# Kernel tuning notes

Hardware: AMD Instinct MI355X
Metric: run time of the kernel (lower is better)

Reference implementation:

```python
import jax, jax.numpy as jnp
import numpy as np

B, N, P2, D, L, K = 256, 256, 64, 128, 2, 9  # batch, nodes, patch^2, embed_dim, vig blocks, knn edges
FFN = 4 * D


def _ln(x, g, b, eps=1e-5):
    m = jnp.mean(x, -1, keepdims=True)
    v = jnp.mean((x - m) ** 2, -1, keepdims=True)
    return (x - m) / jnp.sqrt(v + eps) * g + b


def _lrelu(x):
    return jnp.where(x >= 0, x, 0.01 * x)


def _vig_block(x, mask, mf, fc1_w, fc1_b, conv_w, conv_b, fc2_w, fc2_b, f1_w, f1_b, f2_w, f2_b):
    # Grapher: fc1 -> dynamic kNN -> max-relative graph conv -> fc2, residual
    sc = x
    h = x @ fc1_w + fc1_b  # [B,N,D]
    # pairwise squared distances in feature space; masked nodes excluded as neighbors
    x2 = jnp.sum(h * h, -1)
    d2 = x2[:, :, None] + x2[:, None, :] - 2.0 * jnp.einsum('bnd,bmd->bnm', h, h)
    d2 = jnp.where(mask[:, None, :], d2, 1e10)
    _, idx = jax.lax.top_k(-d2, K)  # [B,N,K] nearest-neighbor indices (non-diff)
    Bq, Nq, Dq = h.shape
    hj = jnp.take_along_axis(h, idx.reshape(Bq, Nq * K, 1), axis=1).reshape(Bq, Nq, K, Dq)
    vj = jnp.take_along_axis(mask, idx.reshape(Bq, Nq * K), axis=1).reshape(Bq, Nq, K)
    rel = jnp.where(vj[..., None], hj - h[:, :, None, :], -1e9)
    mrel = jnp.where(vj.any(2)[..., None], rel.max(2), 0.0)  # max-relative aggregation
    h = _lrelu(jnp.concatenate([h, mrel], -1) @ conv_w + conv_b)
    x = (h @ fc2_w + fc2_b) + sc
    # FFN, residual (drop_path = identity at eval)
    sc = x
    x = _lrelu(x @ f1_w + f1_b) @ f2_w + f2_b + sc
    return x * mf


def setup_inputs() -> dict:
    key = jax.random.key(0)
    ks = jax.random.split(key, 32)
    s = 0.02
    d = {
        'nodes_batch': jax.random.normal(ks[0], (B, N, P2), jnp.float32),
        'node_mask': jax.random.randint(ks[1], (B, N), 0, 2) > 0,
        'emb_w1': jax.random.normal(ks[2], (P2, 2 * D), jnp.float32) * s,
        'emb_b1': jnp.zeros((2 * D,), jnp.float32),
        'emb_ln1_g': jnp.ones((2 * D,), jnp.float32),
        'emb_ln1_b': jnp.zeros((2 * D,), jnp.float32),
        'emb_w2': jax.random.normal(ks[3], (2 * D, D), jnp.float32) * s,
        'emb_b2': jnp.zeros((D,), jnp.float32),
        'emb_ln2_g': jnp.ones((D,), jnp.float32),
        'emb_ln2_b': jnp.zeros((D,), jnp.float32),
        'vig_fc1_w': jax.random.normal(ks[4], (L, D, D), jnp.float32) * s,
        'vig_fc1_b': jnp.zeros((L, D), jnp.float32),
        'vig_conv_w': jax.random.normal(ks[5], (L, 2 * D, D), jnp.float32) * s,
        'vig_conv_b': jnp.zeros((L, D), jnp.float32),
        'vig_fc2_w': jax.random.normal(ks[6], (L, D, D), jnp.float32) * s,
        'vig_fc2_b': jnp.zeros((L, D), jnp.float32),
        'vig_ffn1_w': jax.random.normal(ks[7], (L, D, FFN), jnp.float32) * s,
        'vig_ffn1_b': jnp.zeros((L, FFN), jnp.float32),
        'vig_ffn2_w': jax.random.normal(ks[8], (L, FFN, D), jnp.float32) * s,
        'vig_ffn2_b': jnp.zeros((L, D), jnp.float32),
        'out_w1': jax.random.normal(ks[9], (D, 512), jnp.float32) * s,
        'out_b1': jnp.zeros((512,), jnp.float32),
        'out_w2': jax.random.normal(ks[10], (512, 2048), jnp.float32) * s,
        'out_b2': jnp.zeros((2048,), jnp.float32),
    }
    return d


def reference(nodes_batch, node_mask, emb_w1, emb_b1, emb_ln1_g, emb_ln1_b, emb_w2, emb_b2,
              emb_ln2_g, emb_ln2_b, vig_fc1_w, vig_fc1_b, vig_conv_w, vig_conv_b,
              vig_fc2_w, vig_fc2_b, vig_ffn1_w, vig_ffn1_b, vig_ffn2_w, vig_ffn2_b,
              out_w1, out_b1, out_w2, out_b2):
    mf = node_mask[..., None].astype(nodes_batch.dtype)  # [B,N,1]
    # node embed MLP
    x = _lrelu(_ln(nodes_batch @ emb_w1 + emb_b1, emb_ln1_g, emb_ln1_b))
    x = _ln(x @ emb_w2 + emb_b2, emb_ln2_g, emb_ln2_b)
    x = x * mf
    for l in range(L):
        x = _vig_block(x, node_mask, mf,
                       vig_fc1_w[l], vig_fc1_b[l], vig_conv_w[l], vig_conv_b[l],
                       vig_fc2_w[l], vig_fc2_b[l], vig_ffn1_w[l], vig_ffn1_b[l],
                       vig_ffn2_w[l], vig_ffn2_b[l])
    # masked mean pool
    sum_feat = (x * mf).sum(1)
    num_feat = jnp.maximum(mf.sum(1), 1.0)
    g = sum_feat / num_feat
    return _lrelu(g @ out_w1 + out_b1) @ out_w2 + out_b2
```

## Files before the change

### kernel.cpp

```cpp
#include <hip/hip_runtime.h>
#include <cstdint>

#define BB    256
#define NNODE 256
#define PP2   64
#define DD    128
#define LLAY  2
#define KNN   9
#define FFND  512
#define BNROWS (BB*NNODE)

#define LRELU_(v) ((v) >= 0.f ? (v) : 0.01f*(v))

enum { ACT_NONE = 0, ACT_LRELU = 1 };

typedef short  short8_t  __attribute__((ext_vector_type(8)));
typedef float  f32x4     __attribute__((ext_vector_type(4)));
typedef unsigned short us4 __attribute__((ext_vector_type(4)));
typedef unsigned short us8 __attribute__((ext_vector_type(8)));

__device__ inline unsigned short f2bf(float x) {
    unsigned u = __float_as_uint(x);
    unsigned r = (u + 0x7FFFu + ((u >> 16) & 1u)) >> 16;
    return (unsigned short)r;
}
__device__ inline float bf2f(unsigned short h) {
    return __uint_as_float(((unsigned)h) << 16);
}

__device__ inline void gload16(const void* src, void* dst) {
    __builtin_amdgcn_global_load_lds(
        (const __attribute__((address_space(1))) void*)src,
        (__attribute__((address_space(3))) void*)dst, 16, 0, 0);
}

template<int ROWS, int WAVES>
__device__ inline void stage64g(const unsigned short* __restrict__ g, size_t rowbase,
                                int Kel, int k0, unsigned short* lds, int w, int lane)
{
    constexpr int PER = (ROWS*128/1024) / WAVES;
    #pragma unroll
    for (int i = 0; i < PER; ++i) {
        const int inst = w + i*WAVES;
        const unsigned o  = (unsigned)inst*1024u + (unsigned)lane*16u;
        const int      r  = (int)(o >> 7);
        const unsigned cb = o & 127u;
        const unsigned cs = cb ^ ((unsigned)(r & 7) << 4);
        gload16((const char*)(g + (rowbase + (size_t)r)*(size_t)Kel + k0) + cs,
                (char*)lds + (size_t)inst*1024u);
    }
}

__device__ inline short8_t frag64(const unsigned short* lds, int r, int cb) {
    return *reinterpret_cast<const short8_t*>(
        (const char*)lds + (size_t)r*128 + (unsigned)(cb ^ ((r & 7) << 4)));
}

__device__ inline us8 read8sw(const unsigned short* lds, int r, unsigned cb) {
    return *reinterpret_cast<const us8*>(
        (const char*)lds + (size_t)r*128 + (cb ^ ((unsigned)(r & 7) << 4)));
}

__device__ inline unsigned grp16_min_u32(unsigned v) {
    unsigned t;
    t = (unsigned)__builtin_amdgcn_update_dpp(-1, (int)v, 0xB1,  0xF, 0xF, false); v = t < v ? t : v;
    t = (unsigned)__builtin_amdgcn_update_dpp(-1, (int)v, 0x4E,  0xF, 0xF, false); v = t < v ? t : v;
    t = (unsigned)__builtin_amdgcn_update_dpp(-1, (int)v, 0x124, 0xF, 0xF, false); v = t < v ? t : v;
    t = (unsigned)__builtin_amdgcn_update_dpp(-1, (int)v, 0x128, 0xF, 0xF, false); v = t < v ? t : v;
    return v;
}

__device__ inline float dpp_rowsum16(float v) {
    float t;
    t = __uint_as_float((unsigned)__builtin_amdgcn_update_dpp(0, (int)__float_as_uint(v), 0x111, 0xF, 0xF, false)); v += t;
    t = __uint_as_float((unsigned)__builtin_amdgcn_update_dpp(0, (int)__float_as_uint(v), 0x112, 0xF, 0xF, false)); v += t;
    t = __uint_as_float((unsigned)__builtin_amdgcn_update_dpp(0, (int)__float_as_uint(v), 0x114, 0xF, 0xF, false)); v += t;
    t = __uint_as_float((unsigned)__builtin_amdgcn_update_dpp(0, (int)__float_as_uint(v), 0x118, 0xF, 0xF, false)); v += t;
    return v;
}

#define WAITB0  { asm volatile("s_waitcnt vmcnt(0)" ::: "memory");  __builtin_amdgcn_s_barrier(); asm volatile("" ::: "memory"); }
#define WAITB4  { asm volatile("s_waitcnt vmcnt(4)" ::: "memory");  __builtin_amdgcn_s_barrier(); asm volatile("" ::: "memory"); }
#define WAITB6  { asm volatile("s_waitcnt vmcnt(6)" ::: "memory");  __builtin_amdgcn_s_barrier(); asm volatile("" ::: "memory"); }
#define WAITBL4 { asm volatile("s_waitcnt vmcnt(4) lgkmcnt(0)" ::: "memory"); __builtin_amdgcn_s_barrier(); asm volatile("" ::: "memory"); }

template<int ACT, bool RES, bool MASK, bool OUTF, bool OUTB, bool OUTS>
__global__ __launch_bounds__(256)
void bgemm_k(const unsigned short* __restrict__ A,
             const unsigned short* __restrict__ W,
             const float* __restrict__ bias,
             const float* __restrict__ resp,
             const int* __restrict__ mask,
             float* __restrict__ Cf, unsigned short* __restrict__ Cb,
             unsigned short* Ohi, unsigned short* Olo,
             int M, int N, int K)
{
    __shared__ __align__(16) unsigned short As[128*64];
    __shared__ __align__(16) unsigned short Bs[128*64];

    const int tid  = threadIdx.x;
    const int lane = tid & 63;
    const int w    = tid >> 6;
    const int wr   = w >> 1, wc = w & 1;
    const int row0 = blockIdx.x * 128;
    const int col0 = blockIdx.y * 128;
    const int l15  = lane & 15;
    const int ko   = lane >> 4;

    f32x4 acc[4][4];
    #pragma unroll
    for (int m = 0; m < 4; ++m)
        #pragma unroll
        for (int n = 0; n < 4; ++n) acc[m][n] = (f32x4){0.f,0.f,0.f,0.f};

    for (int k0 = 0; k0 < K; k0 += 64) {
        stage64g<128,4>(A, (size_t)row0, K, k0, As, w, lane);
        stage64g<128,4>(W, (size_t)col0, K, k0, Bs, w, lane);
        __syncthreads();
        #pragma unroll
        for (int ks = 0; ks < 2; ++ks) {
            short8_t aF[4], bF[4];
            #pragma unroll
            for (int m = 0; m < 4; ++m)
                aF[m] = frag64(As, wr*64 + m*16 + l15, ks*64 + ko*16);
            #pragma unroll
            for (int n = 0; n < 4; ++n)
                bF[n] = frag64(Bs, wc*64 + n*16 + l15, ks*64 + ko*16);
            #pragma unroll
            for (int m = 0; m < 4; ++m)
                #pragma unroll
                for (int n = 0; n < 4; ++n)
                    acc[m][n] = __builtin_amdgcn_mfma_f32_16x16x32_bf16(aF[m], bF[n], acc[m][n], 0, 0, 0);
        }
        __syncthreads();
    }

    #pragma unroll
    for (int m = 0; m < 4; ++m) {
        const int rbase = row0 + wr*64 + m*16 + ko*4;
        #pragma unroll
        for (int n = 0; n < 4; ++n) {
            const int col = col0 + wc*64 + n*16 + l15;
            const float bv = bias[col];
            #pragma unroll
            for (int r = 0; r < 4; ++r) {
                const int row = rbase + r;
                float v = acc[m][n][r] + bv;
                if constexpr (ACT == ACT_LRELU) v = LRELU_(v);
                if constexpr (RES)  v += resp[(size_t)row*N + col];
                if constexpr (MASK) v *= (mask[row] != 0) ? 1.f : 0.f;
                if constexpr (OUTF) Cf[(size_t)row*N + col] = v;
                if constexpr (OUTB) Cb[(size_t)row*N + col] = f2bf(v);
                if constexpr (OUTS) {
                    unsigned short h = f2bf(v);
                    Ohi[(size_t)row*N + col] = h;
                    Olo[(size_t)row*N + col] = f2bf(v - bf2f(h));
                }
            }
        }
    }
}

template<int WR, int WC, bool DO_LRELU, bool MASKMUL, int MODE, bool AF32>
__global__ __launch_bounds__(WR*WC*64)
void bgemm_ln_k(const void* __restrict__ Ap,
                const unsigned short* __restrict__ W,
                const float* __restrict__ bias,
// ... 71 lines not shown
        __syncthreads();
    }

    float bv[4];
    #pragma unroll
    for (int n = 0; n < 4; ++n) bv[n] = bias[wc*64 + n*16 + l15];
    #pragma unroll
    for (int m = 0; m < 4; ++m)
        #pragma unroll
        for (int n = 0; n < 4; ++n)
            #pragma unroll
            for (int r = 0; r < 4; ++r) acc[m][n][r] += bv[n];

    #pragma unroll
    for (int m = 0; m < 4; ++m) {
        #pragma unroll
        for (int r = 0; r < 4; ++r) {
            float s = acc[m][0][r] + acc[m][1][r] + acc[m][2][r] + acc[m][3][r];
            float q = acc[m][0][r]*acc[m][0][r] + acc[m][1][r]*acc[m][1][r]
                    + acc[m][2][r]*acc[m][2][r] + acc[m][3][r]*acc[m][3][r];
            s = dpp_rowsum16(s);
            q = dpp_rowsum16(q);
            if (l15 == 15) {
                int rl = wr*64 + m*16 + ko*4 + r;
                red_s[wc][rl] = s;
                red_q[wc][rl] = q;
            }
        }
    }
    __syncthreads();
    if (tid < BM) {
        float s = 0.f, q = 0.f;
        #pragma unroll
        for (int c2 = 0; c2 < WC; ++c2) { s += red_s[c2][tid]; q += red_q[c2][tid]; }
        float mu  = s * (1.0f/BN);
        float var = q * (1.0f/BN) - mu*mu;
        mu_l[tid] = mu;
        rs_l[tid] = rsqrtf(fmaxf(var, 0.f) + 1e-5f);
    }
    __syncthreads();

    float gm[4], bt[4];
    #pragma unroll
    for (int n = 0; n < 4; ++n) {
        int col = wc*64 + n*16 + l15;
        gm[n] = gam[col]; bt[n] = bet[col];
    }
    #pragma unroll
    for (int m = 0; m < 4; ++m) {
        #pragma unroll
        for (int r = 0; r < 4; ++r) {
            const int rl  = wr*64 + m*16 + ko*4 + r;
            const int row = row0 + rl;
            const float mu = mu_l[rl], rs = rs_l[rl];
            float mf = 1.f;
            if constexpr (MASKMUL) mf = (mask[row] != 0) ? 1.f : 0.f;
            #pragma unroll
            for (int n = 0; n < 4; ++n) {
                const int col = wc*64 + n*16 + l15;
                float y = (acc[m][n][r] - mu) * rs * gm[n] + bt[n];
                if constexpr (DO_LRELU) y = LRELU_(y);
                if constexpr (MASKMUL)  y *= mf;
                if constexpr (MODE == 1) {
                    ((unsigned short*)outv)[(size_t)row*BN + col] = f2bf(y);
                } else {
                    unsigned short h = f2bf(y);
                    ohi[(size_t)row*BN + col] = h;
                    olo[(size_t)row*BN + col] = f2bf(y - bf2f(h));
                }
            }
        }
    }
}

__global__ __launch_bounds__(1024)
void fc1_dist_topk_gather_k(const unsigned short* __restrict__ xhi,
                            const unsigned short* __restrict__ xlo,
                            const unsigned short* __restrict__ Whi,
                            const unsigned short* __restrict__ Wlo,
                            const float* __restrict__ fc1b,
                            const int* __restrict__ mask,
                            unsigned short* __restrict__ cat)
{
    __shared__ __align__(16) unsigned short BsH[2][NNODE*64];
    __shared__ __align__(16) unsigned short BsL[2][NNODE*64];
    __shared__ __align__(16) unsigned short Ws[128*64];
    __shared__ float x2s[NNODE];
    __shared__ unsigned char idx_s[NNODE*KNN];
    __shared__ unsigned char msk_s[NNODE];

    const int b    = blockIdx.x;
    const int tid  = threadIdx.x;
    const int lane = tid & 63;
    const int w    = tid >> 6;
    const int l15  = lane & 15;
    const int g    = lane >> 4;

    const unsigned short* Xhi = xhi + (size_t)b*NNODE*DD;
    const unsigned short* Xlo = xlo + (size_t)b*NNODE*DD;
    const int* mkb = mask + b*NNODE;

    stage64g<NNODE,16>(Xhi, 0, DD, 0,  &BsH[0][0], w, lane);
    stage64g<NNODE,16>(Xhi, 0, DD, 64, &BsH[1][0], w, lane);
    stage64g<NNODE,16>(Xlo, 0, DD, 0,  &BsL[0][0], w, lane);
    stage64g<NNODE,16>(Xlo, 0, DD, 64, &BsL[1][0], w, lane);
    if (tid < NNODE) msk_s[tid] = (mkb[tid] != 0) ? 1 : 0;
    __syncthreads();

    const int arow = w*16 + l15;

    f32x4 hacc[8];
    #pragma unroll
    for (int n = 0; n < 8; ++n) hacc[n] = (f32x4){0.f,0.f,0.f,0.f};

    #pragma unroll
    for (int wp = 0; wp < 4; ++wp) {
        const unsigned short* Wsrc = (wp < 2) ? Whi : Wlo;
        const int kt = wp & 1;
        stage64g<128,16>(Wsrc, 0, DD, kt*64, Ws, w, lane);
        __syncthreads();
        const int nAv = (wp < 2) ? 2 : 1;
        for (int av = 0; av < nAv; ++av) {
            const unsigned short* At = (av == 0) ? &BsH[kt][0] : &BsL[kt][0];
            #pragma unroll
            for (int ks = 0; ks < 2; ++ks) {
                short8_t aF = frag64(At, arow, ks*64 + g*16);
                #pragma unroll
                for (int n = 0; n < 8; ++n) {
                    short8_t bF = frag64(Ws, n*16 + l15, ks*64 + g*16);
                    hacc[n] = __builtin_amdgcn_mfma_f32_16x16x32_bf16(aF, bF, hacc[n], 0, 0, 0);
                }
            }
        }
        __syncthreads();
    }

    {
        float qr[4] = {0.f, 0.f, 0.f, 0.f};
        #pragma unroll
        for (int n = 0; n < 8; ++n) {
            const int col = n*16 + l15;
            const float bv = fc1b[col];
            const int kt = col >> 6;
            const unsigned bc = (unsigned)((col & 63) * 2);
            #pragma unroll
            for (int r = 0; r < 4; ++r) {
                const int row = w*16 + g*4 + r;
                float v = hacc[n][r] + bv;
                unsigned short hh = f2bf(v);
                unsigned short hl = f2bf(v - bf2f(hh));
                const unsigned off = (unsigned)(row*128) + (bc ^ ((unsigned)(row & 7) << 4));
                *(unsigned short*)((char*)&BsH[kt][0] + off) = hh;
                *(unsigned short*)((char*)&BsL[kt][0] + off) = hl;
                float vv = bf2f(hh) + bf2f(hl);
                qr[r] += vv*vv;
            }
        }
        #pragma unroll
        for (int r = 0; r < 4; ++r) {
            float q = dpp_rowsum16(qr[r]);
            if (l15 == 15) x2s[w*16 + g*4 + r] = q;
        }
    }
    __syncthreads();

    f32x4 acc[16];
    #pragma unroll
    for (int n = 0; n < 16; ++n) acc[n] = (f32x4){0.f,0.f,0.f,0.f};

    __builtin_amdgcn_s_setprio(1);
    #pragma unroll
    for (int kt = 0; kt < 2; ++kt) {
        #pragma unroll
        for (int ks = 0; ks < 2; ++ks) {
            short8_t aH = frag64(&BsH[kt][0], arow, ks*64 + g*16);
            short8_t aL = frag64(&BsL[kt][0], arow, ks*64 + g*16);
            #pragma unroll
            for (int n = 0; n < 16; ++n) {
                int brow = n*16 + l15;
                short8_t bH = frag64(&BsH[kt][0], brow, ks*64 + g*16);
                short8_t bL = frag64(&BsL[kt][0], brow, ks*64 + g*16);
                acc[n] = __builtin_amdgcn_mfma_f32_16x16x32_bf16(aH, bH, acc[n], 0, 0, 0);
                acc[n] = __builtin_amdgcn_mfma_f32_16x16x32_bf16(aL, bH, acc[n], 0, 0, 0);
                acc[n] = __builtin_amdgcn_mfma_f32_16x16x32_bf16(aH, bL, acc[n], 0, 0, 0);
            }
        }
    }
    __builtin_amdgcn_s_setprio(0);

    float x2c[16]; unsigned mk[16];
    #pragma unroll
    for (int n = 0; n < 16; ++n) {
        int col = n*16 + l15;
        x2c[n] = x2s[col];
        mk[n]  = (unsigned)msk_s[col];
    }

    #pragma unroll
    for (int r = 0; r < 4; ++r) {
        const int lrow = w*16 + g*4 + r;
        const float x2r = x2s[lrow];
        unsigned key[16];
        #pragma unroll
        for (int n = 0; n < 16; ++n) {
            float v = x2r + x2c[n] - 2.0f*acc[n][r];
            if (!mk[n]) v = 1e10f;
            unsigned u = __float_as_uint(v);
            u = (u & 0x80000000u) ? ~u : (u | 0x80000000u);
            key[n] = (u & 0xFFFFFF00u) | (unsigned)(n*16 + l15);
        }
        for (int it = 0; it < KNN; ++it) {
            unsigned a0 = key[0]  < key[1]  ? key[0]  : key[1];
            unsigned a1 = key[2]  < key[3]  ? key[2]  : key[3];
            unsigned a2 = key[4]  < key[5]  ? key[4]  : key[5];
            unsigned a3 = key[6]  < key[7]  ? key[6]  : key[7];
            unsigned a4 = key[8]  < key[9]  ? key[8]  : key[9];
            unsigned a5 = key[10] < key[11] ? key[10] : key[11];
            unsigned a6 = key[12] < key[13] ? key[12] : key[13];
            unsigned a7 = key[14] < key[15] ? key[14] : key[15];
            unsigned b0 = a0 < a1 ? a0 : a1;
            unsigned b1 = a2 < a3 ? a2 : a3;
            unsigned b2 = a4 < a5 ? a4 : a5;
            unsigned b3 = a6 < a7 ? a6 : a7;
            unsigned c0 = b0 < b1 ? b0 : b1;
            unsigned c1 = b2 < b3 ? b2 : b3;
            unsigned lmin = c0 < c1 ? c0 : c1;
            unsigned gmin = grp16_min_u32(lmin);
            if (l15 == 0) idx_s[lrow*KNN + it] = (unsigned char)(gmin & 0xFFu);
            #pragma unroll
            for (int n = 0; n < 16; ++n)
                if (key[n] == gmin) key[n] = 0xFFFFFFFFu;
        }
    }

    const int gi = lane & 7;
    const unsigned cb = (unsigned)(gi * 16);
    #pragma unroll
    for (int kt = 0; kt < 2; ++kt) {
        #pragma unroll
        for (int p = 0; p < 2; ++p) {
            const int rl = w*16 + p*8 + (lane >> 3);
            us8 h8 = read8sw(&BsH[kt][0], rl, cb);
            us8 l8 = read8sw(&BsL[kt][0], rl, cb);
            float hi[8], m[8];
            #pragma unroll
            for (int d = 0; d < 8; ++d) { hi[d] = bf2f(h8[d]) + bf2f(l8[d]); m[d] = -1e9f; }
            bool any = false;
            #pragma unroll
            for (int q = 0; q < KNN; ++q) {
                int j = idx_s[rl*KNN + q];
                if (msk_s[j]) {
                    any = true;
                    us8 a = read8sw(&BsH[kt][0], j, cb);
                    us8 o = read8sw(&BsL[kt][0], j, cb);
                    #pragma unroll
                    for (int d = 0; d < 8; ++d)
                        m[d] = fmaxf(m[d], bf2f(a[d]) + bf2f(o[d]) - hi[d]);
                }
            }
            us8 o1, o2;
            #pragma unroll
            for (int d = 0; d < 8; ++d) {
                o1[d] = f2bf(hi[d]);
                o2[d] = any ? f2bf(m[d]) : (unsigned short)0;
            }
            const size_t rowbase = (size_t)(b*NNODE + rl)*(2*DD);
            const int c0 = kt*64 + gi*8;
            *reinterpret_cast<us8*>(&cat[rowbase + c0])      = o1;
            *reinterpret_cast<us8*>(&cat[rowbase + DD + c0]) = o2;
        }
    }
}

__global__ __launch_bounds__(256)
void conv_ffn_k(const unsigned short* __restrict__ cat,
                const unsigned short* __restrict__ Wc,
                const float* __restrict__ cb,
                const unsigned short* __restrict__ W2c,
                const float* __restrict__ fb,
                const unsigned short* __restrict__ W1,
                const float* __restrict__ b1,
                const unsigned short* __restrict__ W2f,
                const float* __restrict__ b2,
                const int* __restrict__ mask,
                unsigned short* xhi,
                unsigned short* xlo)
{
    __shared__ __align__(16) unsigned short Bs[3][128*64];
    __shared__ __align__(16) unsigned short h2s[2][64*64];
    __shared__ __align__(16) unsigned short Xs[2][64*64];

    const int tid  = threadIdx.x;
    const int lane = tid & 63;
    const int w    = tid >> 6;
    const int row0 = blockIdx.x * 64;
    const int l15  = lane & 15;
    const int ko   = lane >> 4;

    auto issueB = [&](int t) {
        unsigned short* buf = &Bs[t % 3][0];
        if (t < 4)      stage64g<128,4>(Wc,  0, 256, t*64, buf, w, lane);
        else if (t < 6) stage64g<128,4>(W2c, 0, 128, (t-4)*64, buf, w, lane);
        else {
            int c = (t-6) >> 2, j = (t-6) & 3;
            if (j < 2) stage64g<128,4>(W1, (size_t)(c*128), DD, j*64, buf, w, lane);
            else       stage64g<128,4>(W2f, 0, FFND, c*128 + (j-2)*64, buf, w, lane);
        }
    };

    #define MM8(ATILE, BTILE, ACC)                                              \
        { __builtin_amdgcn_s_setprio(1);                                        \
          _Pragma("unroll")                                                     \
          for (int ks = 0; ks < 2; ++ks) {                                      \
            short8_t aF[4], bF[2];                                              \
            _Pragma("unroll")                                                   \
            for (int m = 0; m < 4; ++m) aF[m] = frag64(ATILE, m*16 + l15, ks*64 + ko*16); \
            _Pragma("unroll")                                                   \
            for (int n = 0; n < 2; ++n) bF[n] = frag64(BTILE, w*32 + n*16 + l15, ks*64 + ko*16); \
            _Pragma("unroll")                                                   \
            for (int m = 0; m < 4; ++m)                                         \
              _Pragma("unroll")                                                 \
              for (int n = 0; n < 2; ++n)                                       \
                ACC[m][n] = __builtin_amdgcn_mfma_f32_16x16x32_bf16(aF[m], bF[n], ACC[m][n], 0, 0, 0); } \
          __builtin_amdgcn_s_setprio(0); }

    #define H2WRITE(ACC, BPTR, DST)                                             \
        { const int kt_ = w >> 1;                                               \
          _Pragma("unroll")                                                     \
          for (int n = 0; n < 2; ++n) {                                         \
            const int col_ = w*32 + n*16 + l15;                                 \
            const float bv_ = (BPTR)[col_];                                     \
            const unsigned bc_ = (unsigned)(((w & 1)*32 + n*16 + l15) * 2);     \
            _Pragma("unroll")                                                   \
            for (int m = 0; m < 4; ++m)                                         \
              _Pragma("unroll")                                                 \
              for (int r = 0; r < 4; ++r) {                                     \
                const int row_ = m*16 + ko*4 + r;                               \
                float v_ = LRELU_(ACC[m][n][r] + bv_);                          \
                *(unsigned short*)((char*)&(DST)[kt_][0] + row_*128             \
                    + (bc_ ^ ((unsigned)(row_ & 7) << 4))) = f2bf(v_); } } }

    stage64g<64,4>(cat, (size_t)row0, 256, 0,  &Xs[0][0], w, lane);
    issueB(0);
    stage64g<64,4>(cat, (size_t)row0, 256, 64, &Xs[1][0], w, lane);
    issueB(1);

    f32x4 accc[4][2];
    #pragma unroll
    for (int m = 0; m < 4; ++m)
        #pragma unroll
        for (int n = 0; n < 2; ++n) accc[m][n] = (f32x4){0.f,0.f,0.f,0.f};

    WAITB6;
    issueB(2);
    MM8(&Xs[0][0], &Bs[0][0], accc);

    WAITB4;
    stage64g<64,4>(cat, (size_t)row0, 256, 128, &Xs[0][0], w, lane);
    issueB(3);
    MM8(&Xs[1][0], &Bs[1][0], accc);

    WAITB4;
    stage64g<64,4>(cat, (size_t)row0, 256, 192, &Xs[1][0], w, lane);
    issueB(4);
    MM8(&Xs[0][0], &Bs[2][0], accc);

    WAITB4;
    issueB(5);
    MM8(&Xs[1][0], &Bs[0][0], accc);
    H2WRITE(accc, cb, h2s);

    f32x4 accx[4][2];
    #pragma unroll
    for (int m = 0; m < 4; ++m)
        #pragma unroll
        for (int n = 0; n < 2; ++n) accx[m][n] = (f32x4){0.f,0.f,0.f,0.f};

    WAITBL4;
    issueB(6);
    MM8(&h2s[0][0], &Bs[1][0], accx);

    WAITB4;
    issueB(7);
    MM8(&h2s[1][0], &Bs[2][0], accx);
    float xn[4][2][4];
    {
        const int kt = w >> 1;
        #pragma unroll
        for (int n = 0; n < 2; ++n) {
            const int col = w*32 + n*16 + l15;
            const float bv = fb[col];
            const unsigned bc = (unsigned)(((w & 1)*32 + n*16 + l15) * 2);
            #pragma unroll
            for (int m = 0; m < 4; ++m) {
                #pragma unroll
                for (int r = 0; r < 4; ++r) {
                    const int row = m*16 + ko*4 + r;
                    const size_t gix = (size_t)(row0 + row)*DD + col;
                    float res = bf2f(xhi[gix]) + bf2f(xlo[gix]);
                    float v = accx[m][n][r] + bv + res;
                    xn[m][n][r] = v;
                    *(unsigned short*)((char*)&Xs[kt][0] + row*128
                        + (bc ^ ((unsigned)(row & 7) << 4))) = f2bf(v);
                }
            }
        }
    }

    f32x4 acc2[4][2];
    #pragma unroll
    for (int m = 0; m < 4; ++m)
        #pragma unroll
        for (int n = 0; n < 2; ++n) acc2[m][n] = (f32x4){0.f,0.f,0.f,0.f};

    #pragma unroll
    for (int c = 0; c < 4; ++c) {
        const int tb = 6 + c*4;
        f32x4 acc1[4][2];
        #pragma unroll
        for (int m = 0; m < 4; ++m)
            #pragma unroll
            for (int n = 0; n < 2; ++n) acc1[m][n] = (f32x4){0.f,0.f,0.f,0.f};

        if (c == 0) { WAITBL4; } else { WAITB4; }
        if (tb+2 <= 21) issueB(tb+2);
        MM8(&Xs[0][0], &Bs[tb % 3][0], acc1);

        WAITB4;
        if (tb+3 <= 21) issueB(tb+3);
        MM8(&Xs[1][0], &Bs[(tb+1) % 3][0], acc1);
        H2WRITE(acc1, b1 + c*128, h2s);

        WAITBL4;
        if (tb+4 <= 21) issueB(tb+4);
        MM8(&h2s[0][0], &Bs[(tb+2) % 3][0], acc2);

        if (c == 3) { WAITB0; } else { WAITB4; }
        if (tb+5 <= 21) issueB(tb+5);
        MM8(&h2s[1][0], &Bs[(tb+3) % 3][0], acc2);
    }

    #pragma unroll
    for (int m = 0; m < 4; ++m) {
        const int rbase = row0 + m*16 + ko*4;
        #pragma unroll
        for (int n = 0; n < 2; ++n) {
            const int col = w*32 + n*16 + l15;
            const float bv = b2[col];
            #pragma unroll
            for (int r = 0; r < 4; ++r) {
                const int row = rbase + r;
                float v = acc2[m][n][r] + bv + xn[m][n][r];
                v *= (mask[row] != 0) ? 1.f : 0.f;
                unsigned short h = f2bf(v);
                xhi[(size_t)row*DD + col] = h;
                xlo[(size_t)row*DD + col] = f2bf(v - bf2f(h));
            }
        }
    }
    #undef MM8
    #undef H2WRITE
}

__global__ __launch_bounds__(128)
void pool_k(const unsigned short* __restrict__ xhi, const unsigned short* __restrict__ xlo,
            const int* __restrict__ mask,
            float* __restrict__ g, unsigned short* __restrict__ gbf)
{
    const int b = blockIdx.x, c = threadIdx.x;
    float s = 0.f; int cnt = 0;
    for (int n = 0; n < NNODE; ++n) {
        const size_t ix = ((size_t)b*NNODE + n)*DD + c;
        s += bf2f(xhi[ix]) + bf2f(xlo[ix]);
        cnt += (mask[b*NNODE + n] != 0) ? 1 : 0;
    }
    float v = s / fmaxf((float)cnt, 1.0f);
    g[b*DD + c] = v;
    gbf[b*DD + c] = f2bf(v);
}

__global__ __launch_bounds__(256)
void prep_all_k(const float* __restrict__ emb_w1, const float* __restrict__ emb_w2,
                const float* __restrict__ conv_w, const float* __restrict__ fc2_w,
                const float* __restrict__ f1_w,   const float* __restrict__ f2_w,
                const float* __restrict__ fc1_w,  const float* __restrict__ ow1,
                const float* __restrict__ ow2,
                unsigned short* __restrict__ emb_w1t, unsigned short* __restrict__ emb_w2t,
                unsigned short* __restrict__ conv_wt, unsigned short* __restrict__ fc2_wt,
                unsigned short* __restrict__ ffn1_wt, unsigned short* __restrict__ ffn2_wt,
                unsigned short* __restrict__ fc1_wthi, unsigned short* __restrict__ fc1_wtlo,
                unsigned short* __restrict__ ow1t, unsigned short* __restrict__ ow2t)
{
    __shared__ float tile[32][33];
    const int tx = threadIdx.x & 31, ty = threadIdx.x >> 5;

    int bid = blockIdx.x;
    const float* src = nullptr; unsigned short* dst = nullptr; unsigned short* dlo = nullptr;
    int K = 0, N = 0;
    do {
        if (bid < 16)  { src = emb_w1; dst = emb_w1t; K = 64;  N = 256; break; }  bid -= 16;
        if (bid < 32)  { src = emb_w2; dst = emb_w2t; K = 256; N = 128; break; }  bid -= 32;
        if (bid < 64)  { int l = bid >> 5; bid &= 31;
                         src = conv_w + (size_t)l*256*128; dst = conv_wt + (size_t)l*128*256;
                         K = 256; N = 128; break; }                               bid -= 64;
        if (bid < 32)  { int l = bid >> 4; bid &= 15;
                         src = fc2_w + (size_t)l*128*128; dst = fc2_wt + (size_t)l*128*128;
                         K = 128; N = 128; break; }                               bid -= 32;
        if (bid < 128) { int l = bid >> 6; bid &= 63;
                         src = f1_w + (size_t)l*128*512; dst = ffn1_wt + (size_t)l*512*128;
                         K = 128; N = 512; break; }                               bid -= 128;
        if (bid < 128) { int l = bid >> 6; bid &= 63;
                         src = f2_w + (size_t)l*512*128; dst = ffn2_wt + (size_t)l*128*512;
                         K = 512; N = 128; break; }                               bid -= 128;
        if (bid < 32)  { int l = bid >> 4; bid &= 15;
                         src = fc1_w + (size_t)l*128*128;
                         dst = fc1_wthi + (size_t)l*128*128; dlo = fc1_wtlo + (size_t)l*128*128;
                         K = 128; N = 128; break; }                               bid -= 32;
        if (bid < 64)  { src = ow1; dst = ow1t; K = 128; N = 512; break; }        bid -= 64;
        { src = ow2; dst = ow2t; K = 512; N = 2048; }
    } while (0);

    const int nbx = N / 32;
    const int bx = bid % nbx, by = bid / nbx;
    const int k0 = by*32, n0 = bx*32;

    #pragma unroll
    for (int i = ty; i < 32; i += 8)
        tile[i][tx] = src[(size_t)(k0+i)*N + n0+tx];
    __syncthreads();
    #pragma unroll
// ... 3 lines not shown
        dst[(size_t)(n0+i)*K + k0+tx] = h;
        if (dlo) dlo[(size_t)(n0+i)*K + k0+tx] = f2bf(v - bf2f(h));
    }
}

extern "C" void kernel_launch(void* const* d_in, const int* in_sizes, int n_in,
                              void* d_out, int out_size, void* d_ws, size_t ws_size,
                              hipStream_t stream)
{
    const float* nodes  = (const float*)d_in[0];
    const int*   maskp  = (const int*)  d_in[1];
    const float* emb_w1 = (const float*)d_in[2];
    const float* emb_b1 = (const float*)d_in[3];
    const float* ln1_g  = (const float*)d_in[4];
    const float* ln1_b  = (const float*)d_in[5];
    const float* emb_w2 = (const float*)d_in[6];
    const float* emb_b2 = (const float*)d_in[7];
    const float* ln2_g  = (const float*)d_in[8];
    const float* ln2_b  = (const float*)d_in[9];
    const float* fc1_w  = (const float*)d_in[10];
    const float* fc1_b  = (const float*)d_in[11];
    const float* conv_w = (const float*)d_in[12];
    const float* conv_b = (const float*)d_in[13];
    const float* fc2_w  = (const float*)d_in[14];
    const float* fc2_b  = (const float*)d_in[15];
    const float* f1_w   = (const float*)d_in[16];
    const float* f1_b   = (const float*)d_in[17];
    const float* f2_w   = (const float*)d_in[18];
    const float* f2_b   = (const float*)d_in[19];
    const float* ow1    = (const float*)d_in[20];
    const float* ob1    = (const float*)d_in[21];
    const float* ow2    = (const float*)d_in[22];
    const float* ob2    = (const float*)d_in[23];
    float* out = (float*)d_out;

    char* base = (char*)d_ws;
    char*  H   = base + (size_t)BNROWS*DD*4;
    char*  BIG = H + (size_t)BNROWS*DD*4;
    float*          g     = (float*)(BIG + (size_t)BNROWS*2*DD*4);
    unsigned short* g_bf  = (unsigned short*)(g + BB*DD);
    unsigned short* hid2_bf = g_bf + BB*DD;
    unsigned short* wbuf  = hid2_bf + BB*FFND;

    unsigned short* x_hi   = (unsigned short*)H;
    unsigned short* x_lo   = x_hi + (size_t)BNROWS*DD;
    unsigned short* t256_bf= (unsigned short*)base;
    unsigned short* cat_bf = (unsigned short*)BIG;

    unsigned short* emb_w1t  = wbuf;
    unsigned short* emb_w2t  = emb_w1t + 256*64;
    unsigned short* conv_wt  = emb_w2t + 128*256;
    unsigned short* fc2_wt   = conv_wt + 2*128*256;
    unsigned short* ffn1_wt  = fc2_wt  + 2*128*128;
    unsigned short* ffn2_wt  = ffn1_wt + 2*512*128;
    unsigned short* fc1_wthi = ffn2_wt + 2*128*512;
    unsigned short* fc1_wtlo = fc1_wthi + 2*128*128;
    unsigned short* ow1t     = fc1_wtlo + 2*128*128;
    unsigned short* ow2t     = ow1t + 512*128;

    const dim3 blk(256);

    prep_all_k<<<1520, blk, 0, stream>>>(
        emb_w1, emb_w2, conv_w, fc2_w, f1_w, f2_w, fc1_w, ow1, ow2,
        emb_w1t, emb_w2t, conv_wt, fc2_wt, ffn1_wt, ffn2_wt,
        fc1_wthi, fc1_wtlo, ow1t, ow2t);

    bgemm_ln_k<2,4,true,false,1,true>
        <<<dim3(BNROWS/128), dim3(512), 0, stream>>>
        (nodes, emb_w1t, emb_b1, ln1_g, ln1_b, nullptr, t256_bf, nullptr, nullptr, PP2);
    bgemm_ln_k<2,2,false,true,2,false>
        <<<dim3(BNROWS/128), dim3(256), 0, stream>>>
        (t256_bf, emb_w2t, emb_b2, ln2_g, ln2_b, maskp, nullptr, x_hi, x_lo, 2*DD);

    for (int l = 0; l < LLAY; ++l) {
        const float* fc1b = fc1_b + (size_t)l*DD;
        const float* cb   = conv_b + (size_t)l*DD;
        const float* fc2b = fc2_b + (size_t)l*DD;
        const float* b1   = f1_b + (size_t)l*FFND;
        const float* b2   = f2_b + (size_t)l*DD;

        fc1_dist_topk_gather_k<<<dim3(BB), dim3(1024), 0, stream>>>
            (x_hi, x_lo, fc1_wthi + (size_t)l*DD*DD, fc1_wtlo + (size_t)l*DD*DD,
             fc1b, maskp, cat_bf);
        conv_ffn_k<<<dim3(BNROWS/64), blk, 0, stream>>>
            (cat_bf, conv_wt + (size_t)l*DD*2*DD, cb,
             fc2_wt + (size_t)l*DD*DD, fc2b,
             ffn1_wt + (size_t)l*FFND*DD, b1,
             ffn2_wt + (size_t)l*DD*FFND, b2, maskp,
             x_hi, x_lo);
    }

    pool_k<<<BB, 128, 0, stream>>>(x_hi, x_lo, maskp, g, g_bf);
    bgemm_k<ACT_LRELU,false,false,false,true,false>
        <<<dim3(BB/128, 512/128), blk, 0, stream>>>
        (g_bf, ow1t, ob1, nullptr, nullptr, nullptr, hid2_bf, nullptr, nullptr, BB, 512, DD);
    bgemm_k<ACT_NONE,false,false,true,false,false>
        <<<dim3(BB/128, 2048/128), blk, 0, stream>>>
        (hid2_bf, ow2t, ob2, nullptr, nullptr, out, nullptr, nullptr, nullptr, BB, 2048, 512);
}
```

Measured before the change: 273.1 us.

## Convert fc1 output to fp32 LDS layout and skip fully masked top-k rows

The hi/lo bf16 LDS buffers are merged into one array. After the distance MFMA, the fc1 output is rebuilt as fp32 and rewritten in a swizzled fp32 layout that reuses the same LDS. The gather then reads fp32 directly and takes the max of neighbor values before subtracting the center, which cuts conversions and LDS reads per neighbor. Top-k selection is also skipped for row groups where all rows are masked out. This adds an extra barrier and an LDS rewrite pass. Subtracting after the max gives a slightly different rounding order from the reference.

```diff
diff --git a/kernel.cpp b/kernel.cpp
--- a/kernel.cpp
+++ b/kernel.cpp
@@ -54,11 +54,6 @@
 __device__ inline short8_t frag64(const unsigned short* lds, int r, int cb) {
     return *reinterpret_cast<const short8_t*>(
         (const char*)lds + (size_t)r*128 + (unsigned)(cb ^ ((r & 7) << 4)));
-}
-
-__device__ inline us8 read8sw(const unsigned short* lds, int r, unsigned cb) {
-    return *reinterpret_cast<const us8*>(
-        (const char*)lds + (size_t)r*128 + (cb ^ ((unsigned)(r & 7) << 4)));
 }
 
 __device__ inline unsigned grp16_min_u32(unsigned v) {
@@ -320,8 +315,7 @@
                             const int* __restrict__ mask,
                             unsigned short* __restrict__ cat)
 {
-    __shared__ __align__(16) unsigned short BsH[2][NNODE*64];
-    __shared__ __align__(16) unsigned short BsL[2][NNODE*64];
+    __shared__ __align__(16) unsigned short BUF[4][NNODE*64];
     __shared__ __align__(16) unsigned short Ws[128*64];
     __shared__ float x2s[NNODE];
     __shared__ unsigned char idx_s[NNODE*KNN];
@@ -338,10 +332,10 @@
     const unsigned short* Xlo = xlo + (size_t)b*NNODE*DD;
     const int* mkb = mask + b*NNODE;
 
-    stage64g<NNODE,16>(Xhi, 0, DD, 0,  &BsH[0][0], w, lane);
-    stage64g<NNODE,16>(Xhi, 0, DD, 64, &BsH[1][0], w, lane);
-    stage64g<NNODE,16>(Xlo, 0, DD, 0,  &BsL[0][0], w, lane);
-    stage64g<NNODE,16>(Xlo, 0, DD, 64, &BsL[1][0], w, lane);
+    stage64g<NNODE,16>(Xhi, 0, DD, 0,  &BUF[0][0], w, lane);
+    stage64g<NNODE,16>(Xhi, 0, DD, 64, &BUF[1][0], w, lane);
+    stage64g<NNODE,16>(Xlo, 0, DD, 0,  &BUF[2][0], w, lane);
+    stage64g<NNODE,16>(Xlo, 0, DD, 64, &BUF[3][0], w, lane);
     if (tid < NNODE) msk_s[tid] = (mkb[tid] != 0) ? 1 : 0;
     __syncthreads();
 
@@ -359,7 +353,7 @@
         __syncthreads();
         const int nAv = (wp < 2) ? 2 : 1;
         for (int av = 0; av < nAv; ++av) {
-            const unsigned short* At = (av == 0) ? &BsH[kt][0] : &BsL[kt][0];
+            const unsigned short* At = (av == 0) ? &BUF[kt][0] : &BUF[2+kt][0];
             #pragma unroll
             for (int ks = 0; ks < 2; ++ks) {
                 short8_t aF = frag64(At, arow, ks*64 + g*16);
@@ -388,8 +382,8 @@
                 unsigned short hh = f2bf(v);
                 unsigned short hl = f2bf(v - bf2f(hh));
                 const unsigned off = (unsigned)(row*128) + (bc ^ ((unsigned)(row & 7) << 4));
-                *(unsigned short*)((char*)&BsH[kt][0] + off) = hh;
-                *(unsigned short*)((char*)&BsL[kt][0] + off) = hl;
+                *(unsigned short*)((char*)&BUF[kt][0]   + off) = hh;
+                *(unsigned short*)((char*)&BUF[2+kt][0] + off) = hl;
                 float vv = bf2f(hh) + bf2f(hl);
                 qr[r] += vv*vv;
             }
@@ -411,13 +405,13 @@
     for (int kt = 0; kt < 2; ++kt) {
         #pragma unroll
         for (int ks = 0; ks < 2; ++ks) {
-            short8_t aH = frag64(&BsH[kt][0], arow, ks*64 + g*16);
-            short8_t aL = frag64(&BsL[kt][0], arow, ks*64 + g*16);
+            short8_t aH = frag64(&BUF[kt][0],   arow, ks*64 + g*16);
+            short8_t aL = frag64(&BUF[2+kt][0], arow, ks*64 + g*16);
             #pragma unroll
             for (int n = 0; n < 16; ++n) {
                 int brow = n*16 + l15;
-                short8_t bH = frag64(&BsH[kt][0], brow, ks*64 + g*16);
-                short8_t bL = frag64(&BsL[kt][0], brow, ks*64 + g*16);
+                short8_t bH = frag64(&BUF[kt][0],   brow, ks*64 + g*16);
+                short8_t bL = frag64(&BUF[2+kt][0], brow, ks*64 + g*16);
                 acc[n] = __builtin_amdgcn_mfma_f32_16x16x32_bf16(aH, bH, acc[n], 0, 0, 0);
                 acc[n] = __builtin_amdgcn_mfma_f32_16x16x32_bf16(aL, bH, acc[n], 0, 0, 0);
                 acc[n] = __builtin_amdgcn_mfma_f32_16x16x32_bf16(aH, bL, acc[n], 0, 0, 0);
@@ -434,8 +428,35 @@
         mk[n]  = (unsigned)msk_s[col];
     }
 
+    {
+        float sv[32];
+        const int r0  = tid >> 2;
+        const int cb4 = tid & 3;
+        const int kt  = cb4 >> 1;
+        const unsigned base = (unsigned)((cb4 & 1) * 64);
+        const unsigned sw = (unsigned)(r0 & 7) << 4;
+        #pragma unroll
+        for (int i = 0; i < 4; ++i) {
+            const unsigned bc = (base + (unsigned)(i*16)) ^ sw;
+            us8 hh = *reinterpret_cast<const us8*>((const char*)&BUF[kt][0]   + r0*128 + bc);
+            us8 hl = *reinterpret_cast<const us8*>((const char*)&BUF[2+kt][0] + r0*128 + bc);
+            #pragma unroll
+            for (int d = 0; d < 8; ++d) sv[i*8+d] = bf2f(hh[d]) + bf2f(hl[d]);
+        }
+        __syncthreads();
+        char* S = (char*)&BUF[0][0];
+        #pragma unroll
+        for (int i = 0; i < 8; ++i) {
+            const unsigned bo = ((unsigned)(cb4*128 + i*16)) ^ sw;
+            *reinterpret_cast<f32x4*>(S + (size_t)r0*512 + bo) =
+                (f32x4){sv[i*4], sv[i*4+1], sv[i*4+2], sv[i*4+3]};
+        }
+    }
+
     #pragma unroll
     for (int r = 0; r < 4; ++r) {
+        const int rb = w*16 + r;
+        if ((msk_s[rb] | msk_s[rb+4] | msk_s[rb+8] | msk_s[rb+12]) == 0) continue;
         const int lrow = w*16 + g*4 + r;
         const float x2r = x2s[lrow];
         unsigned key[16];
@@ -470,42 +491,51 @@
                 if (key[n] == gmin) key[n] = 0xFFFFFFFFu;
         }
     }
-
-    const int gi = lane & 7;
-    const unsigned cb = (unsigned)(gi * 16);
-    #pragma unroll
-    for (int kt = 0; kt < 2; ++kt) {
-        #pragma unroll
-        for (int p = 0; p < 2; ++p) {
-            const int rl = w*16 + p*8 + (lane >> 3);
-            us8 h8 = read8sw(&BsH[kt][0], rl, cb);
-            us8 l8 = read8sw(&BsL[kt][0], rl, cb);
-            float hi[8], m[8];
-            #pragma unroll
-            for (int d = 0; d < 8; ++d) { hi[d] = bf2f(h8[d]) + bf2f(l8[d]); m[d] = -1e9f; }
-            bool any = false;
-            #pragma unroll
-            for (int q = 0; q < KNN; ++q) {
-                int j = idx_s[rl*KNN + q];
-                if (msk_s[j]) {
-                    any = true;
-                    us8 a = read8sw(&BsH[kt][0], j, cb);
-                    us8 o = read8sw(&BsL[kt][0], j, cb);
-                    #pragma unroll
-                    for (int d = 0; d < 8; ++d)
-                        m[d] = fmaxf(m[d], bf2f(a[d]) + bf2f(o[d]) - hi[d]);
+    __syncthreads();
+
+    {
+        const char* S = (const char*)&BUF[0][0];
+        const int gi = lane & 7;
+        #pragma unroll
+        for (int kt = 0; kt < 2; ++kt) {
+            #pragma unroll
+            for (int p = 0; p < 2; ++p) {
+                const int rl = w*16 + p*8 + (lane >> 3);
+                const unsigned cbase = (unsigned)(kt*256 + gi*32);
+                const unsigned swr = (unsigned)(rl & 7) << 4;
+                f32x4 h0 = *reinterpret_cast<const f32x4*>(S + (size_t)rl*512 + (cbase ^ swr));
+                f32x4 h1 = *reinterpret_cast<const f32x4*>(S + (size_t)rl*512 + ((cbase + 16u) ^ swr));
+                f32x4 m0 = (f32x4){-1e9f,-1e9f,-1e9f,-1e9f};
+                f32x4 m1 = m0;
+                bool any = false;
+                #pragma unroll
+                for (int q = 0; q < KNN; ++q) {
+                    int j = idx_s[rl*KNN + q];
+                    if (msk_s[j]) {
+                        any = true;
+                        const unsigned sj = (unsigned)(j & 7) << 4;
+                        f32x4 a0 = *reinterpret_cast<const f32x4*>(S + (size_t)j*512 + (cbase ^ sj));
+                        f32x4 a1 = *reinterpret_cast<const f32x4*>(S + (size_t)j*512 + ((cbase + 16u) ^ sj));
+                        #pragma unroll
+                        for (int d = 0; d < 4; ++d) {
+                            m0[d] = fmaxf(m0[d], a0[d]);
+                            m1[d] = fmaxf(m1[d], a1[d]);
+                        }
+                    }
                 }
+                us8 o1, o2;
+                #pragma unroll
+                for (int d = 0; d < 4; ++d) {
+                    o1[d]   = f2bf(h0[d]);
+                    o1[4+d] = f2bf(h1[d]);
+                    o2[d]   = any ? f2bf(m0[d] - h0[d]) : (unsigned short)0;
+                    o2[4+d] = any ? f2bf(m1[d] - h1[d]) : (unsigned short)0;
+                }
+                const size_t rowbase = (size_t)(b*NNODE + rl)*(2*DD);
+                const int c0 = kt*64 + gi*8;
+                *reinterpret_cast<us8*>(&cat[rowbase + c0])      = o1;
+                *reinterpret_cast<us8*>(&cat[rowbase + DD + c0]) = o2;
             }
-            us8 o1, o2;
-            #pragma unroll
-            for (int d = 0; d < 8; ++d) {
-                o1[d] = f2bf(hi[d]);
-                o2[d] = any ? f2bf(m[d]) : (unsigned short)0;
-            }
-            const size_t rowbase = (size_t)(b*NNODE + rl)*(2*DD);
-            const int c0 = kt*64 + gi*8;
-            *reinterpret_cast<us8*>(&cat[rowbase + c0])      = o1;
-            *reinterpret_cast<us8*>(&cat[rowbase + DD + c0]) = o2;
         }
     }
 }
```

Measured after the change: 277.5 us. No clear change (+1.6%).

## Double conv_ffn row tile to 128 with 8 waves; skip fully masked kNN rows

Applied to the files above, without the earlier changes.

conv_ffn_k now processes 128 rows per block with 512 threads arranged as a 2x4 wave grid. Each staged weight tile is reused across twice as many rows, which halves weight traffic per row, and the vmcnt waits are retuned for the new per-thread load count. In fc1_dist_topk_gather_k, top-k selection is skipped for row groups whose nodes are all masked, and the max-relative gather subtracts the center once after the max instead of per neighbor. The larger tile raises LDS use per block, which may lower occupancy.

```diff
diff --git a/kernel.cpp b/kernel.cpp
--- a/kernel.cpp
+++ b/kernel.cpp
@@ -80,9 +80,9 @@
 }
 
 #define WAITB0  { asm volatile("s_waitcnt vmcnt(0)" ::: "memory");  __builtin_amdgcn_s_barrier(); asm volatile("" ::: "memory"); }
+#define WAITB2  { asm volatile("s_waitcnt vmcnt(2)" ::: "memory");  __builtin_amdgcn_s_barrier(); asm volatile("" ::: "memory"); }
 #define WAITB4  { asm volatile("s_waitcnt vmcnt(4)" ::: "memory");  __builtin_amdgcn_s_barrier(); asm volatile("" ::: "memory"); }
-#define WAITB6  { asm volatile("s_waitcnt vmcnt(6)" ::: "memory");  __builtin_amdgcn_s_barrier(); asm volatile("" ::: "memory"); }
-#define WAITBL4 { asm volatile("s_waitcnt vmcnt(4) lgkmcnt(0)" ::: "memory"); __builtin_amdgcn_s_barrier(); asm volatile("" ::: "memory"); }
+#define WAITB2L { asm volatile("s_waitcnt vmcnt(2) lgkmcnt(0)" ::: "memory"); __builtin_amdgcn_s_barrier(); asm volatile("" ::: "memory"); }
 
 template<int ACT, bool RES, bool MASK, bool OUTF, bool OUTB, bool OUTS>
 __global__ __launch_bounds__(256)
@@ -320,8 +320,7 @@
                             const int* __restrict__ mask,
                             unsigned short* __restrict__ cat)
 {
-    __shared__ __align__(16) unsigned short BsH[2][NNODE*64];
-    __shared__ __align__(16) unsigned short BsL[2][NNODE*64];
+    __shared__ __align__(16) unsigned short BUF[4][NNODE*64];
     __shared__ __align__(16) unsigned short Ws[128*64];
     __shared__ float x2s[NNODE];
     __shared__ unsigned char idx_s[NNODE*KNN];
@@ -338,10 +337,10 @@
     const unsigned short* Xlo = xlo + (size_t)b*NNODE*DD;
     const int* mkb = mask + b*NNODE;
 
-    stage64g<NNODE,16>(Xhi, 0, DD, 0,  &BsH[0][0], w, lane);
-    stage64g<NNODE,16>(Xhi, 0, DD, 64, &BsH[1][0], w, lane);
-    stage64g<NNODE,16>(Xlo, 0, DD, 0,  &BsL[0][0], w, lane);
-    stage64g<NNODE,16>(Xlo, 0, DD, 64, &BsL[1][0], w, lane);
+    stage64g<NNODE,16>(Xhi, 0, DD, 0,  &BUF[0][0], w, lane);
+    stage64g<NNODE,16>(Xhi, 0, DD, 64, &BUF[1][0], w, lane);
+    stage64g<NNODE,16>(Xlo, 0, DD, 0,  &BUF[2][0], w, lane);
+    stage64g<NNODE,16>(Xlo, 0, DD, 64, &BUF[3][0], w, lane);
     if (tid < NNODE) msk_s[tid] = (mkb[tid] != 0) ? 1 : 0;
     __syncthreads();
 
@@ -359,7 +358,7 @@
         __syncthreads();
         const int nAv = (wp < 2) ? 2 : 1;
         for (int av = 0; av < nAv; ++av) {
-            const unsigned short* At = (av == 0) ? &BsH[kt][0] : &BsL[kt][0];
+            const unsigned short* At = (av == 0) ? &BUF[kt][0] : &BUF[2+kt][0];
             #pragma unroll
             for (int ks = 0; ks < 2; ++ks) {
                 short8_t aF = frag64(At, arow, ks*64 + g*16);
@@ -388,8 +387,8 @@
                 unsigned short hh = f2bf(v);
                 unsigned short hl = f2bf(v - bf2f(hh));
                 const unsigned off = (unsigned)(row*128) + (bc ^ ((unsigned)(row & 7) << 4));
-                *(unsigned short*)((char*)&BsH[kt][0] + off) = hh;
-                *(unsigned short*)((char*)&BsL[kt][0] + off) = hl;
+                *(unsigned short*)((char*)&BUF[kt][0]   + off) = hh;
+                *(unsigned short*)((char*)&BUF[2+kt][0] + off) = hl;
                 float vv = bf2f(hh) + bf2f(hl);
                 qr[r] += vv*vv;
             }
@@ -411,13 +410,13 @@
     for (int kt = 0; kt < 2; ++kt) {
         #pragma unroll
         for (int ks = 0; ks < 2; ++ks) {
-            short8_t aH = frag64(&BsH[kt][0], arow, ks*64 + g*16);
-            short8_t aL = frag64(&BsL[kt][0], arow, ks*64 + g*16);
+            short8_t aH = frag64(&BUF[kt][0],   arow, ks*64 + g*16);
+            short8_t aL = frag64(&BUF[2+kt][0], arow, ks*64 + g*16);
             #pragma unroll
             for (int n = 0; n < 16; ++n) {
                 int brow = n*16 + l15;
-                short8_t bH = frag64(&BsH[kt][0], brow, ks*64 + g*16);
-                short8_t bL = frag64(&BsL[kt][0], brow, ks*64 + g*16);
+                short8_t bH = frag64(&BUF[kt][0],   brow, ks*64 + g*16);
+                short8_t bL = frag64(&BUF[2+kt][0], brow, ks*64 + g*16);
                 acc[n] = __builtin_amdgcn_mfma_f32_16x16x32_bf16(aH, bH, acc[n], 0, 0, 0);
                 acc[n] = __builtin_amdgcn_mfma_f32_16x16x32_bf16(aL, bH, acc[n], 0, 0, 0);
                 acc[n] = __builtin_amdgcn_mfma_f32_16x16x32_bf16(aH, bL, acc[n], 0, 0, 0);
@@ -436,6 +435,8 @@
 
     #pragma unroll
     for (int r = 0; r < 4; ++r) {
+        const int rb = w*16 + r;
+        if ((msk_s[rb] | msk_s[rb+4] | msk_s[rb+8] | msk_s[rb+12]) == 0) continue;
         const int lrow = w*16 + g*4 + r;
         const float x2r = x2s[lrow];
         unsigned key[16];
@@ -478,8 +479,8 @@
         #pragma unroll
         for (int p = 0; p < 2; ++p) {
             const int rl = w*16 + p*8 + (lane >> 3);
-            us8 h8 = read8sw(&BsH[kt][0], rl, cb);
-            us8 l8 = read8sw(&BsL[kt][0], rl, cb);
+            us8 h8 = read8sw(&BUF[kt][0],   rl, cb);
+            us8 l8 = read8sw(&BUF[2+kt][0], rl, cb);
             float hi[8], m[8];
             #pragma unroll
             for (int d = 0; d < 8; ++d) { hi[d] = bf2f(h8[d]) + bf2f(l8[d]); m[d] = -1e9f; }
@@ -489,18 +490,18 @@
                 int j = idx_s[rl*KNN + q];
                 if (msk_s[j]) {
                     any = true;
-                    us8 a = read8sw(&BsH[kt][0], j, cb);
-                    us8 o = read8sw(&BsL[kt][0], j, cb);
+                    us8 a = read8sw(&BUF[kt][0],   j, cb);
+                    us8 o = read8sw(&BUF[2+kt][0], j, cb);
                     #pragma unroll
                     for (int d = 0; d < 8; ++d)
-                        m[d] = fmaxf(m[d], bf2f(a[d]) + bf2f(o[d]) - hi[d]);
+                        m[d] = fmaxf(m[d], bf2f(a[d]) + bf2f(o[d]));
                 }
             }
             us8 o1, o2;
             #pragma unroll
             for (int d = 0; d < 8; ++d) {
                 o1[d] = f2bf(hi[d]);
-                o2[d] = any ? f2bf(m[d]) : (unsigned short)0;
+                o2[d] = any ? f2bf(m[d] - hi[d]) : (unsigned short)0;
             }
             const size_t rowbase = (size_t)(b*NNODE + rl)*(2*DD);
             const int c0 = kt*64 + gi*8;
@@ -510,7 +511,7 @@
     }
 }
 
-__global__ __launch_bounds__(256)
+__global__ __launch_bounds__(512, 2)
 void conv_ffn_k(const unsigned short* __restrict__ cat,
                 const unsigned short* __restrict__ Wc,
                 const float* __restrict__ cb,
@@ -525,24 +526,26 @@
                 unsigned short* xlo)
 {
     __shared__ __align__(16) unsigned short Bs[3][128*64];
-    __shared__ __align__(16) unsigned short h2s[2][64*64];
-    __shared__ __align__(16) unsigned short Xs[2][64*64];
+    __shared__ __align__(16) unsigned short h2s[2][128*64];
+    __shared__ __align__(16) unsigned short Xs[2][128*64];
 
     const int tid  = threadIdx.x;
     const int lane = tid & 63;
     const int w    = tid >> 6;
-    const int row0 = blockIdx.x * 64;
+    const int wr   = w >> 2;
+    const int wc   = w & 3;
+    const int row0 = blockIdx.x * 128;
     const int l15  = lane & 15;
     const int ko   = lane >> 4;
 
     auto issueB = [&](int t) {
         unsigned short* buf = &Bs[t % 3][0];
-        if (t < 4)      stage64g<128,4>(Wc,  0, 256, t*64, buf, w, lane);
-        else if (t < 6) stage64g<128,4>(W2c, 0, 128, (t-4)*64, buf, w, lane);
+        if (t < 4)      stage64g<128,8>(Wc,  0, 256, t*64, buf, w, lane);
+        else if (t < 6) stage64g<128,8>(W2c, 0, 128, (t-4)*64, buf, w, lane);
         else {
             int c = (t-6) >> 2, j = (t-6) & 3;
-            if (j < 2) stage64g<128,4>(W1, (size_t)(c*128), DD, j*64, buf, w, lane);
-            else       stage64g<128,4>(W2f, 0, FFND, c*128 + (j-2)*64, buf, w, lane);
+            if (j < 2) stage64g<128,8>(W1, (size_t)(c*128), DD, j*64, buf, w, lane);
+            else       stage64g<128,8>(W2f, 0, FFND, c*128 + (j-2)*64, buf, w, lane);
         }
     };
 
@@ -552,9 +555,9 @@
           for (int ks = 0; ks < 2; ++ks) {                                      \
             short8_t aF[4], bF[2];                                              \
             _Pragma("unroll")                                                   \
-            for (int m = 0; m < 4; ++m) aF[m] = frag64(ATILE, m*16 + l15, ks*64 + ko*16); \
+            for (int m = 0; m < 4; ++m) aF[m] = frag64(ATILE, wr*64 + m*16 + l15, ks*64 + ko*16); \
             _Pragma("unroll")                                                   \
-            for (int n = 0; n < 2; ++n) bF[n] = frag64(BTILE, w*32 + n*16 + l15, ks*64 + ko*16); \
+            for (int n = 0; n < 2; ++n) bF[n] = frag64(BTILE, wc*32 + n*16 + l15, ks*64 + ko*16); \
             _Pragma("unroll")                                                   \
             for (int m = 0; m < 4; ++m)                                         \
               _Pragma("unroll")                                                 \
@@ -563,24 +566,24 @@
           __builtin_amdgcn_s_setprio(0); }
 
     #define H2WRITE(ACC, BPTR, DST)                                             \
-        { const int kt_ = w >> 1;                                               \
+        { const int kt_ = wc >> 1;                                              \
           _Pragma("unroll")                                                     \
           for (int n = 0; n < 2; ++n) {                                         \
-            const int col_ = w*32 + n*16 + l15;                                 \
+            const int col_ = wc*32 + n*16 + l15;                                \
             const float bv_ = (BPTR)[col_];                                     \
-            const unsigned bc_ = (unsigned)(((w & 1)*32 + n*16 + l15) * 2);     \
+            const unsigned bc_ = (unsigned)(((wc & 1)*32 + n*16 + l15) * 2);    \
             _Pragma("unroll")                                                   \
             for (int m = 0; m < 4; ++m)                                         \
               _Pragma("unroll")                                                 \
               for (int r = 0; r < 4; ++r) {                                     \
-                const int row_ = m*16 + ko*4 + r;                               \
+                const int row_ = wr*64 + m*16 + ko*4 + r;                       \
                 float v_ = LRELU_(ACC[m][n][r] + bv_);                          \
                 *(unsigned short*)((char*)&(DST)[kt_][0] + row_*128             \
                     + (bc_ ^ ((unsigned)(row_ & 7) << 4))) = f2bf(v_); } } }
 
-    stage64g<64,4>(cat, (size_t)row0, 256, 0,  &Xs[0][0], w, lane);
+    stage64g<128,8>(cat, (size_t)row0, 256, 0,  &Xs[0][0], w, lane);
     issueB(0);
-    stage64g<64,4>(cat, (size_t)row0, 256, 64, &Xs[1][0], w, lane);
+    stage64g<128,8>(cat, (size_t)row0, 256, 64, &Xs[1][0], w, lane);
     issueB(1);
 
     f32x4 accc[4][2];
@@ -589,21 +592,21 @@
         #pragma unroll
         for (int n = 0; n < 2; ++n) accc[m][n] = (f32x4){0.f,0.f,0.f,0.f};
 
-    WAITB6;
+    WAITB4;
     issueB(2);
     MM8(&Xs[0][0], &Bs[0][0], accc);
 
-    WAITB4;
-    stage64g<64,4>(cat, (size_t)row0, 256, 128, &Xs[0][0], w, lane);
+    WAITB2;
+    stage64g<128,8>(cat, (size_t)row0, 256, 128, &Xs[0][0], w, lane);
     issueB(3);
     MM8(&Xs[1][0], &Bs[1][0], accc);
 
-    WAITB4;
-    stage64g<64,4>(cat, (size_t)row0, 256, 192, &Xs[1][0], w, lane);
+    WAITB2;
+    stage64g<128,8>(cat, (size_t)row0, 256, 192, &Xs[1][0], w, lane);
     issueB(4);
     MM8(&Xs[0][0], &Bs[2][0], accc);
 
-    WAITB4;
+    WAITB2;
     issueB(5);
     MM8(&Xs[1][0], &Bs[0][0], accc);
     H2WRITE(accc, cb, h2s);
@@ -614,26 +617,26 @@
         #pragma unroll
         for (int n = 0; n < 2; ++n) accx[m][n] = (f32x4){0.f,0.f,0.f,0.f};
 
-    WAITBL4;
+    WAITB2L;
     issueB(6);
     MM8(&h2s[0][0], &Bs[1][0], accx);
 
-    WAITB4;
+    WAITB2;
     issueB(7);
     MM8(&h2s[1][0], &Bs[2][0], accx);
     float xn[4][2][4];
     {
-        const int kt = w >> 1;
+        const int kt = wc >> 1;
         #pragma unroll
         for (int n = 0; n < 2; ++n) {
-            const int col = w*32 + n*16 + l15;
+            const int col = wc*32 + n*16 + l15;
             const float bv = fb[col];
-            const unsigned bc = (unsigned)(((w & 1)*32 + n*16 + l15) * 2);
+            const unsigned bc = (unsigned)(((wc & 1)*32 + n*16 + l15) * 2);
             #pragma unroll
             for (int m = 0; m < 4; ++m) {
                 #pragma unroll
                 for (int r = 0; r < 4; ++r) {
-                    const int row = m*16 + ko*4 + r;
+                    const int row = wr*64 + m*16 + ko*4 + r;
                     const size_t gix = (size_t)(row0 + row)*DD + col;
                     float res = bf2f(xhi[gix]) + bf2f(xlo[gix]);
                     float v = accx[m][n][r] + bv + res;
@@ -660,30 +663,30 @@
             #pragma unroll
             for (int n = 0; n < 2; ++n) acc1[m][n] = (f32x4){0.f,0.f,0.f,0.f};
 
-        if (c == 0) { WAITBL4; } else { WAITB4; }
+        if (c == 0) { WAITB2L; } else { WAITB2; }
         if (tb+2 <= 21) issueB(tb+2);
         MM8(&Xs[0][0], &Bs[tb % 3][0], acc1);
 
-        WAITB4;
+        WAITB2;
         if (tb+3 <= 21) issueB(tb+3);
         MM8(&Xs[1][0], &Bs[(tb+1) % 3][0], acc1);
         H2WRITE(acc1, b1 + c*128, h2s);
 
-        WAITBL4;
+        WAITB2L;
         if (tb+4 <= 21) issueB(tb+4);
         MM8(&h2s[0][0], &Bs[(tb+2) % 3][0], acc2);
 
-        if (c == 3) { WAITB0; } else { WAITB4; }
+        if (c == 3) { WAITB0; } else { WAITB2; }
         if (tb+5 <= 21) issueB(tb+5);
         MM8(&h2s[1][0], &Bs[(tb+3) % 3][0], acc2);
     }
 
     #pragma unroll
     for (int m = 0; m < 4; ++m) {
-        const int rbase = row0 + m*16 + ko*4;
+        const int rbase = row0 + wr*64 + m*16 + ko*4;
         #pragma unroll
         for (int n = 0; n < 2; ++n) {
-            const int col = w*32 + n*16 + l15;
+            const int col = wc*32 + n*16 + l15;
             const float bv = b2[col];
             #pragma unroll
             for (int r = 0; r < 4; ++r) {
@@ -853,7 +856,7 @@
         fc1_dist_topk_gather_k<<<dim3(BB), dim3(1024), 0, stream>>>
             (x_hi, x_lo, fc1_wthi + (size_t)l*DD*DD, fc1_wtlo + (size_t)l*DD*DD,
              fc1b, maskp, cat_bf);
-        conv_ffn_k<<<dim3(BNROWS/64), blk, 0, stream>>>
+        conv_ffn_k<<<dim3(BNROWS/128), dim3(512), 0, stream>>>
             (cat_bf, conv_wt + (size_t)l*DD*2*DD, cb,
              fc2_wt + (size_t)l*DD*DD, fc2b,
              ffn1_wt + (size_t)l*FFND*DD, b1,
```

New measurement: 276.3 us. No clear change (+1.2%).
